# Kernel optimization log

Hardware: AMD Instinct MI355X
Metric: run time of the kernel (lower is better)

Reference implementation:

```python
import jax, jax.numpy as jnp
import numpy as np

EPS = 1e-6
K_HOPS = 2  # SGConv K


def setup_inputs() -> dict:
    key = jax.random.key(0)
    k1, k2, k3, k4 = jax.random.split(key, 4)
    B, Kk, C, T = 32, 8, 64, 250
    E, H = 4096, 128
    x = jax.random.normal(k1, (B, Kk, C, T), dtype=jnp.float32)
    edge_index = jax.random.randint(k2, (2, E), 0, C, dtype=jnp.int64)
    edge_weights = jax.random.uniform(k3, (E,), dtype=jnp.float32)
    W = jax.random.normal(k4, (H, Kk * T), dtype=jnp.float32) * 0.02
    b = jnp.zeros((H,), dtype=jnp.float32)
    return {"x": x, "edge_index": edge_index, "edge_weights": edge_weights, "W": W, "b": b}


def reference(x, edge_index, edge_weights, W, b):
    B, Kk, C, T = x.shape
    N = C  # nodes
    x = x.reshape(B, N, Kk * T)  # (B, N, F)

    # clamp non-positive edge weights to epsilon (mirrors in-place .data clamp)
    w = jnp.where(edge_weights <= 0, EPS, edge_weights)

    # gcn_norm with self loops (fill value 1.0)
    src, dst = edge_index[0], edge_index[1]
    loop = jnp.arange(N, dtype=edge_index.dtype)
    src = jnp.concatenate([src, loop])
    dst = jnp.concatenate([dst, loop])
    w = jnp.concatenate([w, jnp.ones((N,), w.dtype)])
    deg = jnp.zeros((N,), w.dtype).at[dst].add(w)
    dinv = jnp.where(deg > 0, deg ** -0.5, jnp.zeros_like(deg))
    norm = dinv[src] * w * dinv[dst]  # (E+N,)

    # K hops of gather -> weight -> scatter-add aggregation
    for _ in range(K_HOPS):
        msg = x[:, src, :] * norm[None, :, None]        # (B, E+N, F)
        x = jnp.zeros_like(x).at[:, dst, :].add(msg)    # (B, N, F)

    # final linear: y = x @ W^T + b
    return jnp.einsum('bnf,hf->bnh', x, W) + b
```

## Files before the change

### kernel.cpp

```cpp
#include <hip/hip_runtime.h>
#include <hip/hip_bf16.h>

#define EPSW 1e-6f

typedef __attribute__((ext_vector_type(4))) float floatx4;
typedef __attribute__((ext_vector_type(4))) unsigned int uintx4;
typedef __attribute__((ext_vector_type(8))) short shortx8;

__device__ __forceinline__ unsigned short f2bf(float f) {
    unsigned int u = __float_as_uint(f);
    u = (u + 0x7fffu + ((u >> 16) & 1u)) >> 16;
    return (unsigned short)u;
}

__device__ __forceinline__ unsigned int pk2(float lo, float hi) {
    return (unsigned int)f2bf(lo) | ((unsigned int)f2bf(hi) << 16);
}

__device__ __forceinline__ void gl_lds16(const void* g, void* l) {
    __builtin_amdgcn_global_load_lds(
        (const __attribute__((address_space(1))) unsigned int*)g,
        (__attribute__((address_space(3))) unsigned int*)l, 16, 0, 0);
}

__global__ __launch_bounds__(512) void prep(const float* __restrict__ W,
                                            const int* __restrict__ ei,
                                            const float* __restrict__ ew,
                                            unsigned short* __restrict__ wt,
                                            float* __restrict__ Mt) {
    __shared__ float sA[4096 + 128];
    const int bid = blockIdx.x;
    const int t   = threadIdx.x;

    if (bid < 16) {
#pragma unroll
        for (int i = 0; i < 4; ++i) {
            const int G  = bid * 2048 + i * 512 + t;
            const int kg = G >> 7;
            const int h  = G & 127;
            const int k  = kg * 8;
            floatx4 v0 = (floatx4){0.f, 0.f, 0.f, 0.f};
            floatx4 v1 = (floatx4){0.f, 0.f, 0.f, 0.f};
            if (k < 2000) {
                v0 = *(const floatx4*)(W + (size_t)h * 2000 + k);
                v1 = *(const floatx4*)(W + (size_t)h * 2000 + k + 4);
            }
            unsigned short* p = wt + ((size_t)kg * 128 + h) * 8;
            p[0] = f2bf(v0.x); p[1] = f2bf(v0.y); p[2] = f2bf(v0.z); p[3] = f2bf(v0.w);
            p[4] = f2bf(v1.x); p[5] = f2bf(v1.y); p[6] = f2bf(v1.z); p[7] = f2bf(v1.w);
        }
    } else {
        const int bb = bid - 16;
        float* A    = sA;
        float* deg  = sA + 4096;
        float* dinv = deg + 64;
        if (t < 64) deg[t] = 1.0f;
        for (int i = t; i < 4096; i += 512) A[i] = 0.0f;
        __syncthreads();
        const int* srcp = ei;
        const int* dstp = ei + 4096;
#pragma unroll
        for (int i = 0; i < 8; ++i) {
            const int e = i * 512 + t;
            float w = ew[e];
            w = (w <= 0.0f) ? EPSW : w;
            atomicAdd(&deg[dstp[e]], w);
        }
        __syncthreads();
        if (t < 64) dinv[t] = 1.0f / sqrtf(deg[t]);
        __syncthreads();
#pragma unroll
        for (int i = 0; i < 8; ++i) {
            const int e = i * 512 + t;
            float w = ew[e];
            w = (w <= 0.0f) ? EPSW : w;
            const int s = srcp[e], d = dstp[e];
            atomicAdd(&A[d * 64 + s], dinv[s] * w * dinv[d]);
        }
        if (t < 64) atomicAdd(&A[t * 64 + t], dinv[t] * dinv[t]);
        __syncthreads();
        const int c  = t & 63;
        const int n0 = bb * 16 + (t >> 6);
        const int n1 = n0 + 8;
        float s0 = 0.0f, s1 = 0.0f;
#pragma unroll 8
        for (int k = 0; k < 64; ++k) {
            const float akc = A[k * 64 + c];
            s0 += A[n0 * 64 + k] * akc;
            s1 += A[n1 * 64 + k] * akc;
        }
        Mt[c * 64 + n0] = s0;
        Mt[c * 64 + n1] = s1;
    }
}

__global__ __launch_bounds__(256) void gemm_lds(
        const float* __restrict__ x,
        const unsigned short* __restrict__ wt,
        float* __restrict__ zp) {
    __shared__ __align__(16) unsigned char smem[2][24576];
    const int t    = threadIdx.x;
    const int wave = t >> 6, lane = t & 63;
    const int m = lane & 15, q = lane >> 4;
    const int bid   = blockIdx.x;
    const int ks    = bid >> 5;
    const int rbase = (bid & 31) * 64;
    const int kg0   = ks * 32;

    const int kgl = lane >> 3;
    const int rr0 = wave * 8 + (lane & 7);

    floatx4 acc[4][2];
#pragma unroll
    for (int rt = 0; rt < 4; ++rt)
#pragma unroll
        for (int hh = 0; hh < 2; ++hh)
            acc[rt][hh] = (floatx4){0.f, 0.f, 0.f, 0.f};

    floatx4 va0, va1, vb0, vb1;

#define LOAD_A(c)                                                             \
    {                                                                         \
        const int k_ = ks * 256 + (c) * 64 + kgl * 8;                         \
        const float* px_ = x + (size_t)(rbase + rr0) * 2000 + k_;             \
        if (k_ < 2000) {                                                      \
            va0 = *(const floatx4*)px_;                                       \
            va1 = *(const floatx4*)(px_ + 4);                                 \
            vb0 = *(const floatx4*)(px_ + 64000);                             \
            vb1 = *(const floatx4*)(px_ + 64004);                             \
        } else {                                                              \
            va0 = va1 = vb0 = vb1 = (floatx4){0.f, 0.f, 0.f, 0.f};            \
        }                                                                     \
    }

#define WRITE_A(c)                                                            \
    {                                                                         \
        unsigned char* sb_ = smem[(c) & 1];                                   \
        uintx4 g0_, g1_;                                                      \
        g0_.x = pk2(va0.x, va0.y); g0_.y = pk2(va0.z, va0.w);                 \
        g0_.z = pk2(va1.x, va1.y); g0_.w = pk2(va1.z, va1.w);                 \
        g1_.x = pk2(vb0.x, vb0.y); g1_.y = pk2(vb0.z, vb0.w);                 \
        g1_.z = pk2(vb1.x, vb1.y); g1_.w = pk2(vb1.z, vb1.w);                 \
        *(uintx4*)(sb_ + kgl * 1024 + rr0 * 16) = g0_;                        \
        *(uintx4*)(sb_ + kgl * 1024 + (rr0 + 32) * 16) = g1_;                 \
    }

#define ISSUE_B(c)                                                            \
    {                                                                         \
        unsigned char* sb_ = smem[(c) & 1];                                   \
        const int ckg_ = kg0 + (c) * 8;                                       \
        for (int j = wave; j < 16; j += 4) {                                  \
            const int kb_ = j >> 1, hf_ = j & 1;                              \
            gl_lds16(wt + ((size_t)(ckg_ + kb_) * 128 + hf_ * 64 + lane) * 8, \
                     sb_ + 8192 + kb_ * 2048 + hf_ * 1024);                   \
        }                                                                     \
    }

    LOAD_A(0);
    ISSUE_B(0);
    for (int c = 0; c < 4; ++c) {
        __builtin_amdgcn_s_waitcnt(0);
        WRITE_A(c);
        if (c < 3) {
            LOAD_A(c + 1);
            ISSUE_B(c + 1);
        }
        __syncthreads();
        const unsigned char* sb = smem[c & 1];
#pragma unroll
        for (int p = 0; p < 2; ++p) {
            shortx8 a[4];
#pragma unroll
            for (int rt = 0; rt < 4; ++rt)
                a[rt] = *(const shortx8*)(sb + (p * 4 + q) * 1024 + (rt * 16 + m) * 16);
            shortx8 bb[2];
#pragma unroll
            for (int hh = 0; hh < 2; ++hh)
                bb[hh] = *(const shortx8*)(sb + 8192 + (p * 4 + q) * 2048 +
                                           ((wave + hh * 4) * 16 + m) * 16);
#pragma unroll
            for (int rt = 0; rt < 4; ++rt)
#pragma unroll
                for (int hh = 0; hh < 2; ++hh)
                    acc[rt][hh] = __builtin_amdgcn_mfma_f32_16x16x32_bf16(
                        a[rt], bb[hh], acc[rt][hh], 0, 0, 0);
        }
        __syncthreads();
    }
#undef LOAD_A
#undef WRITE_A
#undef ISSUE_B

#pragma unroll
    for (int rt = 0; rt < 4; ++rt)
#pragma unroll
        for (int hh = 0; hh < 2; ++hh) {
            const int h = (wave + hh * 4) * 16 + m;
#pragma unroll
            for (int v = 0; v < 4; ++v) {
                const int row = rbase + rt * 16 + q * 4 + v;
                zp[((size_t)ks * 2048 + row) * 128 + h] = acc[rt][hh][v];
            }
        }
}

__global__ __launch_bounds__(256) void apply_M(const float* __restrict__ zp,
                                               const float* __restrict__ Mtg,
                                               const float* __restrict__ bias,
                                               float* __restrict__ y) {
    __shared__ float Ms[4096];
    __shared__ float zs[64][16];
    const int b  = blockIdx.x;
    const int hc = blockIdx.y;
    const int t  = threadIdx.x;
#pragma unroll
    for (int i = 0; i < 16; ++i) Ms[i * 256 + t] = Mtg[i * 256 + t];
#pragma unroll
    for (int i = 0; i < 4; ++i) {
        const int idx = i * 256 + t;
        const int mr = idx >> 4, hh = idx & 15;
        float s = 0.0f;
#pragma unroll
        for (int ks = 0; ks < 8; ++ks)
            s += zp[((size_t)ks * 2048 + b * 64 + mr) * 128 + hc * 16 + hh];
        zs[mr][hh] = s;
    }
    __syncthreads();
    const int h  = t & 15;
    const int n0 = (t >> 4) * 4;
    const float bv = bias[hc * 16 + h];
    float s0 = bv, s1 = bv, s2 = bv, s3 = bv;
#pragma unroll
    for (int mm = 0; mm < 64; ++mm) {
        const float zv = zs[mm][h];
        s0 += Ms[mm * 64 + n0 + 0] * zv;
        s1 += Ms[mm * 64 + n0 + 1] * zv;
        s2 += Ms[mm * 64 + n0 + 2] * zv;
        s3 += Ms[mm * 64 + n0 + 3] * zv;
    }
    float* yp = y + (size_t)b * 8192 + (size_t)n0 * 128 + hc * 16 + h;
    yp[0]   = s0;
    yp[128] = s1;
    yp[256] = s2;
    yp[384] = s3;
}

extern "C" void kernel_launch(void* const* d_in, const int* in_sizes, int n_in,
                              void* d_out, int out_size, void* d_ws, size_t ws_size,
                              hipStream_t stream) {
    const float* x    = (const float*)d_in[0];
    const int*   ei   = (const int*)d_in[1];
    const float* ew   = (const float*)d_in[2];
    const float* W    = (const float*)d_in[3];
    const float* bias = (const float*)d_in[4];
    float* y = (float*)d_out;

    float* zp = (float*)d_ws;
    float* Mt = zp + 2097152;
    unsigned short* wt = (unsigned short*)(Mt + 4096);

    prep<<<20, 512, 0, stream>>>(W, ei, ew, wt, Mt);
    gemm_lds<<<256, 256, 0, stream>>>(x, wt, zp);
    apply_M<<<dim3(32, 8), 256, 0, stream>>>(zp, Mt, bias, y);
}
```

Before: 93.45 us.

## Fuse node-mixing matrix into GEMM epilogue with split-bf16 MFMA and atomics

Removes the apply_M kernel and the large per-split partial workspace. Each GEMM block now multiplies its partial result by the propagation matrix M in its epilogue, using hi/lo bf16 splitting on MFMA to keep near-fp32 accuracy, and atomically adds into y. The prep kernel gains extra blocks that initialise y with the bias. This saves one launch and about 8 MB of partial-sum traffic. In exchange it adds float atomics (8-way contention per output, nondeterministic summation order) and extra LDS and MFMA work per block.

```diff
diff --git a/kernel.cpp b/kernel.cpp
--- a/kernel.cpp
+++ b/kernel.cpp
@@ -4,6 +4,7 @@
 #define EPSW 1e-6f
 
 typedef __attribute__((ext_vector_type(4))) float floatx4;
+typedef __attribute__((ext_vector_type(2))) unsigned int uintx2;
 typedef __attribute__((ext_vector_type(4))) unsigned int uintx4;
 typedef __attribute__((ext_vector_type(8))) short shortx8;
 
@@ -13,6 +14,10 @@
     return (unsigned short)u;
 }
 
+__device__ __forceinline__ float bf2f(unsigned short b) {
+    return __uint_as_float((unsigned int)b << 16);
+}
+
 __device__ __forceinline__ unsigned int pk2(float lo, float hi) {
     return (unsigned int)f2bf(lo) | ((unsigned int)f2bf(hi) << 16);
 }
@@ -26,8 +31,10 @@
 __global__ __launch_bounds__(512) void prep(const float* __restrict__ W,
                                             const int* __restrict__ ei,
                                             const float* __restrict__ ew,
+                                            const float* __restrict__ bias,
                                             unsigned short* __restrict__ wt,
-                                            float* __restrict__ Mt) {
+                                            float* __restrict__ Mt,
+                                            float* __restrict__ y) {
     __shared__ float sA[4096 + 128];
     const int bid = blockIdx.x;
     const int t   = threadIdx.x;
@@ -49,7 +56,7 @@
             p[0] = f2bf(v0.x); p[1] = f2bf(v0.y); p[2] = f2bf(v0.z); p[3] = f2bf(v0.w);
             p[4] = f2bf(v1.x); p[5] = f2bf(v1.y); p[6] = f2bf(v1.z); p[7] = f2bf(v1.w);
         }
-    } else {
+    } else if (bid < 20) {
         const int bb = bid - 16;
         float* A    = sA;
         float* deg  = sA + 4096;
@@ -91,20 +98,30 @@
         }
         Mt[c * 64 + n0] = s0;
         Mt[c * 64 + n1] = s1;
-    }
-}
-
-__global__ __launch_bounds__(256) void gemm_lds(
+    } else {
+        const floatx4 bv = *(const floatx4*)(bias + (t & 31) * 4);
+#pragma unroll
+        for (int i = 0; i < 16; ++i) {
+            const int idx4 = (bid - 20) * 8192 + i * 512 + t;
+            *(floatx4*)(y + (size_t)idx4 * 4) = bv;
+        }
+    }
+}
+
+__global__ __launch_bounds__(256) void gemm_fused(
         const float* __restrict__ x,
         const unsigned short* __restrict__ wt,
-        float* __restrict__ zp) {
+        const float* __restrict__ Mtg,
+        float* __restrict__ y) {
     __shared__ __align__(16) unsigned char smem[2][24576];
+    __shared__ __align__(16) unsigned char mg[16384];
     const int t    = threadIdx.x;
     const int wave = t >> 6, lane = t & 63;
     const int m = lane & 15, q = lane >> 4;
     const int bid   = blockIdx.x;
     const int ks    = bid >> 5;
-    const int rbase = (bid & 31) * 64;
+    const int bb    = bid & 31;
+    const int rbase = bb * 64;
     const int kg0   = ks * 32;
 
     const int kgl = lane >> 3;
@@ -158,6 +175,30 @@
 
     LOAD_A(0);
     ISSUE_B(0);
+
+#pragma unroll
+    for (int s = 0; s < 2; ++s) {
+        const int g  = t * 2 + s;
+        const int kg = g >> 6, n = g & 63;
+        float v[8];
+#pragma unroll
+        for (int j = 0; j < 8; ++j) v[j] = Mtg[(kg * 8 + j) * 64 + n];
+        unsigned short hb[8];
+#pragma unroll
+        for (int j = 0; j < 8; ++j) hb[j] = f2bf(v[j]);
+        uintx4 wh, wl;
+        wh.x = (unsigned)hb[0] | ((unsigned)hb[1] << 16);
+        wh.y = (unsigned)hb[2] | ((unsigned)hb[3] << 16);
+        wh.z = (unsigned)hb[4] | ((unsigned)hb[5] << 16);
+        wh.w = (unsigned)hb[6] | ((unsigned)hb[7] << 16);
+        wl.x = pk2(v[0] - bf2f(hb[0]), v[1] - bf2f(hb[1]));
+        wl.y = pk2(v[2] - bf2f(hb[2]), v[3] - bf2f(hb[3]));
+        wl.z = pk2(v[4] - bf2f(hb[4]), v[5] - bf2f(hb[5]));
+        wl.w = pk2(v[6] - bf2f(hb[6]), v[7] - bf2f(hb[7]));
+        *(uintx4*)(mg + g * 16)        = wh;
+        *(uintx4*)(mg + 8192 + g * 16) = wl;
+    }
+
     for (int c = 0; c < 4; ++c) {
         __builtin_amdgcn_s_waitcnt(0);
         WRITE_A(c);
@@ -173,17 +214,17 @@
 #pragma unroll
             for (int rt = 0; rt < 4; ++rt)
                 a[rt] = *(const shortx8*)(sb + (p * 4 + q) * 1024 + (rt * 16 + m) * 16);
-            shortx8 bb[2];
+            shortx8 bbf[2];
 #pragma unroll
             for (int hh = 0; hh < 2; ++hh)
-                bb[hh] = *(const shortx8*)(sb + 8192 + (p * 4 + q) * 2048 +
-                                           ((wave + hh * 4) * 16 + m) * 16);
+                bbf[hh] = *(const shortx8*)(sb + 8192 + (p * 4 + q) * 2048 +
+                                            ((wave + hh * 4) * 16 + m) * 16);
 #pragma unroll
             for (int rt = 0; rt < 4; ++rt)
 #pragma unroll
                 for (int hh = 0; hh < 2; ++hh)
                     acc[rt][hh] = __builtin_amdgcn_mfma_f32_16x16x32_bf16(
-                        a[rt], bb[hh], acc[rt][hh], 0, 0, 0);
+                        a[rt], bbf[hh], acc[rt][hh], 0, 0, 0);
         }
         __syncthreads();
     }
@@ -191,58 +232,78 @@
 #undef WRITE_A
 #undef ISSUE_B
 
-#pragma unroll
-    for (int rt = 0; rt < 4; ++rt)
+    unsigned char* zhi = smem[0];
+    unsigned char* zlo = smem[1];
+#pragma unroll
+    for (int rt = 0; rt < 4; ++rt) {
+        const int kg  = rt * 2 + (q >> 1);
+        const int off = (q & 1) * 8;
 #pragma unroll
         for (int hh = 0; hh < 2; ++hh) {
             const int h = (wave + hh * 4) * 16 + m;
+            const floatx4 a = acc[rt][hh];
+            const unsigned short h0 = f2bf(a.x), h1 = f2bf(a.y),
+                                 h2 = f2bf(a.z), h3 = f2bf(a.w);
+            uintx2 wh, wl;
+            wh.x = (unsigned)h0 | ((unsigned)h1 << 16);
+            wh.y = (unsigned)h2 | ((unsigned)h3 << 16);
+            wl.x = pk2(a.x - bf2f(h0), a.y - bf2f(h1));
+            wl.y = pk2(a.z - bf2f(h2), a.w - bf2f(h3));
+            const int base = (kg * 129 + h) * 16 + off;
+            *(uintx2*)(zhi + base) = wh;
+            *(uintx2*)(zlo + base) = wl;
+        }
+    }
+    __syncthreads();
+
+    floatx4 acc2[4][2];
+#pragma unroll
+    for (int nt = 0; nt < 4; ++nt)
+#pragma unroll
+        for (int hh = 0; hh < 2; ++hh)
+            acc2[nt][hh] = (floatx4){0.f, 0.f, 0.f, 0.f};
+
+#pragma unroll
+    for (int kst = 0; kst < 2; ++kst) {
+        shortx8 ah[4], al[4];
+#pragma unroll
+        for (int nt = 0; nt < 4; ++nt) {
+            const int ga = ((kst * 4 + q) * 64 + nt * 16 + m) * 16;
+            ah[nt] = *(const shortx8*)(mg + ga);
+            al[nt] = *(const shortx8*)(mg + 8192 + ga);
+        }
+        shortx8 bh[2], bl[2];
+#pragma unroll
+        for (int hh = 0; hh < 2; ++hh) {
+            const int gb = ((kst * 4 + q) * 129 + (wave + hh * 4) * 16 + m) * 16;
+            bh[hh] = *(const shortx8*)(zhi + gb);
+            bl[hh] = *(const shortx8*)(zlo + gb);
+        }
+#pragma unroll
+        for (int nt = 0; nt < 4; ++nt)
+#pragma unroll
+            for (int hh = 0; hh < 2; ++hh) {
+                acc2[nt][hh] = __builtin_amdgcn_mfma_f32_16x16x32_bf16(
+                    ah[nt], bh[hh], acc2[nt][hh], 0, 0, 0);
+                acc2[nt][hh] = __builtin_amdgcn_mfma_f32_16x16x32_bf16(
+                    ah[nt], bl[hh], acc2[nt][hh], 0, 0, 0);
+                acc2[nt][hh] = __builtin_amdgcn_mfma_f32_16x16x32_bf16(
+                    al[nt], bh[hh], acc2[nt][hh], 0, 0, 0);
+            }
+    }
+
+    float* yb = y + (size_t)bb * 8192;
+#pragma unroll
+    for (int nt = 0; nt < 4; ++nt)
+#pragma unroll
+        for (int hh = 0; hh < 2; ++hh) {
+            const int h = (wave + hh * 4) * 16 + m;
 #pragma unroll
             for (int v = 0; v < 4; ++v) {
-                const int row = rbase + rt * 16 + q * 4 + v;
-                zp[((size_t)ks * 2048 + row) * 128 + h] = acc[rt][hh][v];
+                const int n = nt * 16 + q * 4 + v;
+                atomicAdd(yb + n * 128 + h, acc2[nt][hh][v]);
             }
         }
-}
-
-__global__ __launch_bounds__(256) void apply_M(const float* __restrict__ zp,
-                                               const float* __restrict__ Mtg,
-                                               const float* __restrict__ bias,
-                                               float* __restrict__ y) {
-    __shared__ float Ms[4096];
-    __shared__ float zs[64][16];
-    const int b  = blockIdx.x;
-    const int hc = blockIdx.y;
-    const int t  = threadIdx.x;
-#pragma unroll
-    for (int i = 0; i < 16; ++i) Ms[i * 256 + t] = Mtg[i * 256 + t];
-#pragma unroll
-    for (int i = 0; i < 4; ++i) {
-        const int idx = i * 256 + t;
-        const int mr = idx >> 4, hh = idx & 15;
-        float s = 0.0f;
-#pragma unroll
-        for (int ks = 0; ks < 8; ++ks)
-            s += zp[((size_t)ks * 2048 + b * 64 + mr) * 128 + hc * 16 + hh];
-        zs[mr][hh] = s;
-    }
-    __syncthreads();
-    const int h  = t & 15;
-    const int n0 = (t >> 4) * 4;
-    const float bv = bias[hc * 16 + h];
-    float s0 = bv, s1 = bv, s2 = bv, s3 = bv;
-#pragma unroll
-    for (int mm = 0; mm < 64; ++mm) {
-        const float zv = zs[mm][h];
-        s0 += Ms[mm * 64 + n0 + 0] * zv;
-        s1 += Ms[mm * 64 + n0 + 1] * zv;
-        s2 += Ms[mm * 64 + n0 + 2] * zv;
-        s3 += Ms[mm * 64 + n0 + 3] * zv;
-    }
-    float* yp = y + (size_t)b * 8192 + (size_t)n0 * 128 + hc * 16 + h;
-    yp[0]   = s0;
-    yp[128] = s1;
-    yp[256] = s2;
-    yp[384] = s3;
 }
 
 extern "C" void kernel_launch(void* const* d_in, const int* in_sizes, int n_in,
@@ -255,11 +316,9 @@
     const float* bias = (const float*)d_in[4];
     float* y = (float*)d_out;
 
-    float* zp = (float*)d_ws;
-    float* Mt = zp + 2097152;
+    float* Mt = (float*)d_ws;
     unsigned short* wt = (unsigned short*)(Mt + 4096);
 
-    prep<<<20, 512, 0, stream>>>(W, ei, ew, wt, Mt);
-    gemm_lds<<<256, 256, 0, stream>>>(x, wt, zp);
-    apply_M<<<dim3(32, 8), 256, 0, stream>>>(zp, Mt, bias, y);
-}
+    prep<<<28, 512, 0, stream>>>(W, ei, ew, bias, wt, Mt, y);
+    gemm_fused<<<256, 256, 0, stream>>>(x, wt, Mt, y);
+}
```

Measured after the change: 95.05 us. Within noise of the previous version (+1.7%).

## Fuse prep and GEMM into one kernel, converting W to bf16 inline

Applied to the files above, without the earlier changes.

Removes the separate prep kernel that pre-converted W to a bf16 tiled layout. The GEMM kernel now loads fp32 W directly and converts it to bf16 while staging it into LDS, and the first four blocks compute the propagation matrix M. Blocks grow to 512 threads, with each wave handling one 16-column slice of H. This saves a kernel launch and the write and re-read of the bf16 W copy. In exchange every GEMM block re-reads and re-converts W in fp32, and the async global-to-LDS loads are dropped.

```diff
diff --git a/kernel.cpp b/kernel.cpp
--- a/kernel.cpp
+++ b/kernel.cpp
@@ -17,42 +17,27 @@
     return (unsigned int)f2bf(lo) | ((unsigned int)f2bf(hi) << 16);
 }
 
-__device__ __forceinline__ void gl_lds16(const void* g, void* l) {
-    __builtin_amdgcn_global_load_lds(
-        (const __attribute__((address_space(1))) unsigned int*)g,
-        (__attribute__((address_space(3))) unsigned int*)l, 16, 0, 0);
-}
-
-__global__ __launch_bounds__(512) void prep(const float* __restrict__ W,
-                                            const int* __restrict__ ei,
-                                            const float* __restrict__ ew,
-                                            unsigned short* __restrict__ wt,
-                                            float* __restrict__ Mt) {
-    __shared__ float sA[4096 + 128];
+__device__ __forceinline__ uintx4 pk8(floatx4 a, floatx4 b) {
+    uintx4 r;
+    r.x = pk2(a.x, a.y); r.y = pk2(a.z, a.w);
+    r.z = pk2(b.x, b.y); r.w = pk2(b.z, b.w);
+    return r;
+}
+
+__global__ __launch_bounds__(512) void gemm_mt(
+        const float* __restrict__ x,
+        const float* __restrict__ W,
+        const int* __restrict__ ei,
+        const float* __restrict__ ew,
+        float* __restrict__ zp,
+        float* __restrict__ Mt) {
+    __shared__ __align__(16) unsigned char smem[2][24576];
     const int bid = blockIdx.x;
     const int t   = threadIdx.x;
 
-    if (bid < 16) {
-#pragma unroll
-        for (int i = 0; i < 4; ++i) {
-            const int G  = bid * 2048 + i * 512 + t;
-            const int kg = G >> 7;
-            const int h  = G & 127;
-            const int k  = kg * 8;
-            floatx4 v0 = (floatx4){0.f, 0.f, 0.f, 0.f};
-            floatx4 v1 = (floatx4){0.f, 0.f, 0.f, 0.f};
-            if (k < 2000) {
-                v0 = *(const floatx4*)(W + (size_t)h * 2000 + k);
-                v1 = *(const floatx4*)(W + (size_t)h * 2000 + k + 4);
-            }
-            unsigned short* p = wt + ((size_t)kg * 128 + h) * 8;
-            p[0] = f2bf(v0.x); p[1] = f2bf(v0.y); p[2] = f2bf(v0.z); p[3] = f2bf(v0.w);
-            p[4] = f2bf(v1.x); p[5] = f2bf(v1.y); p[6] = f2bf(v1.z); p[7] = f2bf(v1.w);
-        }
-    } else {
-        const int bb = bid - 16;
-        float* A    = sA;
-        float* deg  = sA + 4096;
+    if (bid < 4) {
+        float* A    = (float*)smem;
+        float* deg  = A + 4096;
         float* dinv = deg + 64;
         if (t < 64) deg[t] = 1.0f;
         for (int i = t; i < 4096; i += 512) A[i] = 0.0f;
@@ -80,7 +65,7 @@
         if (t < 64) atomicAdd(&A[t * 64 + t], dinv[t] * dinv[t]);
         __syncthreads();
         const int c  = t & 63;
-        const int n0 = bb * 16 + (t >> 6);
+        const int n0 = bid * 16 + (t >> 6);
         const int n1 = n0 + 8;
         float s0 = 0.0f, s1 = 0.0f;
 #pragma unroll 8
@@ -91,117 +76,85 @@
         }
         Mt[c * 64 + n0] = s0;
         Mt[c * 64 + n1] = s1;
-    }
-}
-
-__global__ __launch_bounds__(256) void gemm_lds(
-        const float* __restrict__ x,
-        const unsigned short* __restrict__ wt,
-        float* __restrict__ zp) {
-    __shared__ __align__(16) unsigned char smem[2][24576];
-    const int t    = threadIdx.x;
+        return;
+    }
+
+    const int g     = bid - 4;
+    const int ks    = g >> 5;
+    const int bb    = g & 31;
+    const int rbase = bb * 64;
+    const int kbase = ks * 256;
+
     const int wave = t >> 6, lane = t & 63;
     const int m = lane & 15, q = lane >> 4;
-    const int bid   = blockIdx.x;
-    const int ks    = bid >> 5;
-    const int rbase = (bid & 31) * 64;
-    const int kg0   = ks * 32;
-
-    const int kgl = lane >> 3;
-    const int rr0 = wave * 8 + (lane & 7);
-
-    floatx4 acc[4][2];
-#pragma unroll
-    for (int rt = 0; rt < 4; ++rt)
-#pragma unroll
-        for (int hh = 0; hh < 2; ++hh)
-            acc[rt][hh] = (floatx4){0.f, 0.f, 0.f, 0.f};
-
-    floatx4 va0, va1, vb0, vb1;
-
-#define LOAD_A(c)                                                             \
+    const int kq = t & 7;
+    const int rw = t >> 3;
+
+    floatx4 acc[4];
+#pragma unroll
+    for (int rt = 0; rt < 4; ++rt) acc[rt] = (floatx4){0.f, 0.f, 0.f, 0.f};
+
+    floatx4 va0, va1, wb00, wb01, wb10, wb11;
+
+#define LOADC(c)                                                              \
     {                                                                         \
-        const int k_ = ks * 256 + (c) * 64 + kgl * 8;                         \
-        const float* px_ = x + (size_t)(rbase + rr0) * 2000 + k_;             \
+        const int k_ = kbase + (c) * 64 + kq * 8;                             \
         if (k_ < 2000) {                                                      \
-            va0 = *(const floatx4*)px_;                                       \
-            va1 = *(const floatx4*)(px_ + 4);                                 \
-            vb0 = *(const floatx4*)(px_ + 64000);                             \
-            vb1 = *(const floatx4*)(px_ + 64004);                             \
+            const float* pa_ = x + (size_t)(rbase + rw) * 2000 + k_;          \
+            const float* p0_ = W + (size_t)rw * 2000 + k_;                    \
+            const float* p1_ = W + (size_t)(rw + 64) * 2000 + k_;             \
+            va0  = *(const floatx4*)pa_;  va1  = *(const floatx4*)(pa_ + 4);  \
+            wb00 = *(const floatx4*)p0_;  wb01 = *(const floatx4*)(p0_ + 4);  \
+            wb10 = *(const floatx4*)p1_;  wb11 = *(const floatx4*)(p1_ + 4);  \
         } else {                                                              \
-            va0 = va1 = vb0 = vb1 = (floatx4){0.f, 0.f, 0.f, 0.f};            \
+            va0 = va1 = wb00 = wb01 = wb10 = wb11 =                           \
+                (floatx4){0.f, 0.f, 0.f, 0.f};                                \
         }                                                                     \
     }
 
-#define WRITE_A(c)                                                            \
+#define WRITEC(c)                                                             \
     {                                                                         \
         unsigned char* sb_ = smem[(c) & 1];                                   \
-        uintx4 g0_, g1_;                                                      \
-        g0_.x = pk2(va0.x, va0.y); g0_.y = pk2(va0.z, va0.w);                 \
-        g0_.z = pk2(va1.x, va1.y); g0_.w = pk2(va1.z, va1.w);                 \
-        g1_.x = pk2(vb0.x, vb0.y); g1_.y = pk2(vb0.z, vb0.w);                 \
-        g1_.z = pk2(vb1.x, vb1.y); g1_.w = pk2(vb1.z, vb1.w);                 \
-        *(uintx4*)(sb_ + kgl * 1024 + rr0 * 16) = g0_;                        \
-        *(uintx4*)(sb_ + kgl * 1024 + (rr0 + 32) * 16) = g1_;                 \
-    }
-
-#define ISSUE_B(c)                                                            \
-    {                                                                         \
-        unsigned char* sb_ = smem[(c) & 1];                                   \
-        const int ckg_ = kg0 + (c) * 8;                                       \
-        for (int j = wave; j < 16; j += 4) {                                  \
-            const int kb_ = j >> 1, hf_ = j & 1;                              \
-            gl_lds16(wt + ((size_t)(ckg_ + kb_) * 128 + hf_ * 64 + lane) * 8, \
-                     sb_ + 8192 + kb_ * 2048 + hf_ * 1024);                   \
-        }                                                                     \
-    }
-
-    LOAD_A(0);
-    ISSUE_B(0);
+        *(uintx4*)(sb_ + kq * 1024 + rw * 16)               = pk8(va0, va1);  \
+        *(uintx4*)(sb_ + 8192 + kq * 2048 + rw * 16)        = pk8(wb00, wb01);\
+        *(uintx4*)(sb_ + 8192 + kq * 2048 + (rw + 64) * 16) = pk8(wb10, wb11);\
+    }
+
+    LOADC(0);
     for (int c = 0; c < 4; ++c) {
-        __builtin_amdgcn_s_waitcnt(0);
-        WRITE_A(c);
-        if (c < 3) {
-            LOAD_A(c + 1);
-            ISSUE_B(c + 1);
-        }
+        WRITEC(c);
+        if (c < 3) LOADC(c + 1);
         __syncthreads();
         const unsigned char* sb = smem[c & 1];
 #pragma unroll
         for (int p = 0; p < 2; ++p) {
+            const int kgq = p * 4 + q;
             shortx8 a[4];
 #pragma unroll
             for (int rt = 0; rt < 4; ++rt)
-                a[rt] = *(const shortx8*)(sb + (p * 4 + q) * 1024 + (rt * 16 + m) * 16);
-            shortx8 bb[2];
-#pragma unroll
-            for (int hh = 0; hh < 2; ++hh)
-                bb[hh] = *(const shortx8*)(sb + 8192 + (p * 4 + q) * 2048 +
-                                           ((wave + hh * 4) * 16 + m) * 16);
+                a[rt] = *(const shortx8*)(sb + kgq * 1024 + (rt * 16 + m) * 16);
+            const shortx8 bf = *(const shortx8*)(sb + 8192 + kgq * 2048 +
+                                                 (wave * 16 + m) * 16);
 #pragma unroll
             for (int rt = 0; rt < 4; ++rt)
-#pragma unroll
-                for (int hh = 0; hh < 2; ++hh)
-                    acc[rt][hh] = __builtin_amdgcn_mfma_f32_16x16x32_bf16(
-                        a[rt], bb[hh], acc[rt][hh], 0, 0, 0);
-        }
-        __syncthreads();
-    }
-#undef LOAD_A
-#undef WRITE_A
-#undef ISSUE_B
-
-#pragma unroll
-    for (int rt = 0; rt < 4; ++rt)
-#pragma unroll
-        for (int hh = 0; hh < 2; ++hh) {
-            const int h = (wave + hh * 4) * 16 + m;
-#pragma unroll
-            for (int v = 0; v < 4; ++v) {
-                const int row = rbase + rt * 16 + q * 4 + v;
-                zp[((size_t)ks * 2048 + row) * 128 + h] = acc[rt][hh][v];
-            }
-        }
+                acc[rt] = __builtin_amdgcn_mfma_f32_16x16x32_bf16(
+                    a[rt], bf, acc[rt], 0, 0, 0);
+        }
+        __syncthreads();
+    }
+#undef LOADC
+#undef WRITEC
+
+    float* zslice = zp + ((size_t)ks * 2048 + rbase) * 128;
+    const int h = wave * 16 + m;
+#pragma unroll
+    for (int rt = 0; rt < 4; ++rt) {
+#pragma unroll
+        for (int v = 0; v < 4; ++v) {
+            const int n = rt * 16 + q * 4 + v;
+            zslice[n * 128 + h] = acc[rt][v];
+        }
+    }
 }
 
 __global__ __launch_bounds__(256) void apply_M(const float* __restrict__ zp,
@@ -257,9 +210,7 @@
 
     float* zp = (float*)d_ws;
     float* Mt = zp + 2097152;
-    unsigned short* wt = (unsigned short*)(Mt + 4096);
-
-    prep<<<20, 512, 0, stream>>>(W, ei, ew, wt, Mt);
-    gemm_lds<<<256, 256, 0, stream>>>(x, wt, zp);
+
+    gemm_mt<<<260, 512, 0, stream>>>(x, W, ei, ew, zp, Mt);
     apply_M<<<dim3(32, 8), 256, 0, stream>>>(zp, Mt, bias, y);
 }
```

After: 88.61 us. 5.2% less time.
